# Performance work log

Measured on AMD Instinct MI355X. Metric: run time of the kernel, lower is better.

Reference implementation:

```python
import jax, jax.numpy as jnp
import numpy as np

D_MODEL = 256
N_HEADS = 8
HEAD_DIM = D_MODEL // N_HEADS


def setup_inputs() -> dict:
    key = jax.random.key(0)
    k1, k2, k3, k4, k5, k6, k7 = jax.random.split(key, 7)
    B, T, N, D = 4, 32, 32, D_MODEL
    x = jax.random.normal(k1, (B, T, N, D), dtype=jnp.float32)
    bias_features = jax.random.normal(k2, (B, T, N, N, D), dtype=jnp.float32)
    # alive mask, mostly True so rows are rarely fully masked
    mask = jax.random.uniform(k3, (B, T, N)) < 0.9
    s = 1.0 / np.sqrt(D)
    w_qkv = jax.random.normal(k4, (D, 3 * D), dtype=jnp.float32) * s
    b_qkv = jnp.zeros((3 * D,), dtype=jnp.float32)
    w_proj = jax.random.normal(k5, (D, D), dtype=jnp.float32) * s
    b_proj = jnp.zeros((D,), dtype=jnp.float32)
    return {"x": x, "bias_features": bias_features, "mask": mask,
            "w_qkv": w_qkv, "b_qkv": b_qkv, "w_proj": w_proj, "b_proj": b_proj}


def reference(x, bias_features, mask, w_qkv, b_qkv, w_proj, b_proj):
    B, T, N, D = x.shape
    H, Dh = N_HEADS, D // N_HEADS
    Bt = B * T
    xf = x.reshape(Bt, N, D)
    qkv = xf @ w_qkv + b_qkv                       # (Bt, N, 3D)
    q, k, v = jnp.split(qkv, 3, axis=-1)
    q = q.reshape(Bt, N, H, Dh)
    k = k.reshape(Bt, N, H, Dh)
    v = v.reshape(Bt, N, H, Dh)
    b_geo = bias_features.reshape(Bt, N, N, H, Dh)
    k_pair = k[:, None] + b_geo                    # (Bt, N, N, H, Dh)
    v_pair = v[:, None] + b_geo
    # scores: (Bt, H, N, N)
    scores = jnp.einsum('bihd,bijhd->bhij', q, k_pair) * (Dh ** -0.5)
    mask_flat = mask.reshape(Bt, 1, 1, N)
    scores = jnp.where(mask_flat, scores, -jnp.inf)
    max_scores = jnp.max(scores, axis=-1, keepdims=True)
    is_nan_row = max_scores == -jnp.inf
    scores_safe = jnp.where(is_nan_row, 0.0, scores)
    attn = jax.nn.softmax(scores_safe, axis=-1)
    attn = jnp.where(is_nan_row, 0.0, attn)
    out = jnp.einsum('bhij,bijhd->bihd', attn, v_pair).reshape(Bt, N, D)
    out = out.reshape(B, T, N, D)
    return out @ w_proj + b_proj
```

## Files before the change

### kernel.cpp

```cpp
#include <hip/hip_runtime.h>
#include <math.h>

typedef __attribute__((ext_vector_type(8))) short bf16x8;
typedef __attribute__((ext_vector_type(4))) short bf16x4;
typedef __attribute__((ext_vector_type(4))) float f32x4;

__device__ inline ushort f2bf(float f) {
    union { float f; uint u; } v; v.f = f;
    uint u = v.u;
    return (ushort)((u + 0x7fff + ((u >> 16) & 1)) >> 16);
}
__device__ inline float bf2f(ushort u) {
    union { uint u; float f; } v; v.u = ((uint)u) << 16; return v.f;
}

template<int BM, int BN, int WGM, int WGN, int MODE>
__global__ __launch_bounds__(WGM * WGN * 64) void gemm_fused(
    const void* __restrict__ Ap, const float* __restrict__ Bw, int ldb,
    const float* __restrict__ bias,
    void* __restrict__ C0, void* __restrict__ C1, void* __restrict__ C2,
    int K, int N)
{
    constexpr int BK = 32;
    constexpr int NT = WGM * WGN * 64;
    constexpr int WM = BM / (WGM * 16);
    constexpr int WN = BN / (WGN * 16);

    __shared__ ushort As[BM * BK];
    __shared__ ushort Bs[BN * BK];

    const int tid = threadIdx.x;
    const int lane = tid & 63, wid = tid >> 6;
    const int wm = wid / WGN, wn = wid % WGN;
    const int row0 = blockIdx.y * BM, col0 = blockIdx.x * BN;
    const int frow = lane & 15, fg = lane >> 4;

    f32x4 acc[WM][WN] = {};

    for (int k0 = 0; k0 < K; k0 += BK) {
        if constexpr (MODE == 0) {
            #pragma unroll
            for (int ci = tid; ci < BM * 8; ci += NT) {
                int r = ci >> 3, kq = ci & 7, g = kq >> 1;
                float4 v = *(const float4*)((const float*)Ap + (size_t)(row0 + r) * K + k0 + kq * 4);
                bf16x4 o;
                o[0] = (short)f2bf(v.x); o[1] = (short)f2bf(v.y);
                o[2] = (short)f2bf(v.z); o[3] = (short)f2bf(v.w);
                *(bf16x4*)&As[r * 32 + ((g ^ ((r >> 1) & 3)) << 3) + (kq & 1) * 4] = o;
            }
        } else {
            #pragma unroll
            for (int ci = tid; ci < BM * 4; ci += NT) {
                int r = ci >> 2, g = ci & 3;
                bf16x8 v = *(const bf16x8*)((const ushort*)Ap + (size_t)(row0 + r) * K + k0 + g * 8);
                *(bf16x8*)&As[r * 32 + ((g ^ ((r >> 1) & 3)) << 3)] = v;
            }
        }
        #pragma unroll
        for (int ci = tid; ci < BN * 8; ci += NT) {
            int kk = ci & 31, n4 = ci >> 5;
            float4 v = *(const float4*)&Bw[(size_t)(k0 + kk) * ldb + col0 + n4 * 4];
            float vv[4] = {v.x, v.y, v.z, v.w};
            #pragma unroll
            for (int e = 0; e < 4; ++e) {
                int n = n4 * 4 + e;
                Bs[n * 32 + (((kk >> 3) ^ ((n >> 1) & 3)) << 3) + (kk & 7)] = f2bf(vv[e]);
            }
        }
        __syncthreads();

        bf16x8 af[WM], bfr[WN];
        #pragma unroll
        for (int m = 0; m < WM; ++m) {
            int r = (wm * WM + m) * 16 + frow;
            af[m] = *(const bf16x8*)&As[r * 32 + ((fg ^ ((r >> 1) & 3)) << 3)];
        }
        #pragma unroll
        for (int n = 0; n < WN; ++n) {
            int r = (wn * WN + n) * 16 + frow;
            bfr[n] = *(const bf16x8*)&Bs[r * 32 + ((fg ^ ((r >> 1) & 3)) << 3)];
        }
        #pragma unroll
        for (int m = 0; m < WM; ++m)
            #pragma unroll
            for (int n = 0; n < WN; ++n)
                acc[m][n] = __builtin_amdgcn_mfma_f32_16x16x32_bf16(
                    af[m], bfr[n], acc[m][n], 0, 0, 0);
        __syncthreads();
    }

    #pragma unroll
    for (int n = 0; n < WN; ++n) {
        int gcol = col0 + (wn * WN + n) * 16 + frow;
        float bv = bias[gcol];
        if constexpr (MODE == 0) {
            int b = gcol >> 8, c = gcol & 255;
            ushort* dst = (b == 0) ? (ushort*)C0 : (b == 1) ? (ushort*)C1 : (ushort*)C2;
            #pragma unroll
            for (int m = 0; m < WM; ++m) {
                int grow0 = row0 + (wm * WM + m) * 16 + fg * 4;
                #pragma unroll
                for (int r = 0; r < 4; ++r)
                    dst[(size_t)(grow0 + r) * 256 + c] = f2bf(acc[m][n][r] + bv);
            }
        } else {
            float* dst = (float*)C0;
            #pragma unroll
            for (int m = 0; m < WM; ++m) {
                int grow0 = row0 + (wm * WM + m) * 16 + fg * 4;
                #pragma unroll
                for (int r = 0; r < 4; ++r)
                    dst[(size_t)(grow0 + r) * N + gcol] = acc[m][n][r] + bv;
            }
        }
    }
}

__global__ __launch_bounds__(256) void relattn_kernel(
    const ushort* __restrict__ qb, const ushort* __restrict__ kb,
    const ushort* __restrict__ vb, const float* __restrict__ bias,
    const int* __restrict__ mask, ushort* __restrict__ attn_out)
{
    __shared__ ushort bias_lds[8192];
    __shared__ float p_lds[256];

    const int blk = blockIdx.x;
    const int bt = blk >> 5;
    const int tid = threadIdx.x;
    const float* bsrc = bias + (size_t)blk * 8192;

    #pragma unroll
    for (int it = 0; it < 8; ++it) {
        int idx4 = it * 256 + tid;
        float4 v = *(const float4*)(bsrc + (size_t)idx4 * 4);
        int j = idx4 >> 6;
        int c = (idx4 & 63) >> 1;
        int half = idx4 & 1;
        bf16x4 o;
        o[0] = (short)f2bf(v.x); o[1] = (short)f2bf(v.y);
        o[2] = (short)f2bf(v.z); o[3] = (short)f2bf(v.w);
        *(bf16x4*)&bias_lds[j * 256 + ((c ^ (j & 7)) << 3) + half * 4] = o;
    }
    __syncthreads();

    const int j = tid & 31, h = tid >> 5;
    const ushort* qrow = qb + (size_t)blk * 256 + h * 32;
    const ushort* krow = kb + (size_t)(bt * 32 + j) * 256 + h * 32;

    float s = 0.f;
    #pragma unroll
    for (int it = 0; it < 4; ++it) {
        bf16x8 q8 = *(const bf16x8*)(qrow + it * 8);
        bf16x8 k8 = *(const bf16x8*)(krow + it * 8);
        int c = h * 4 + it;
        bf16x8 b8 = *(const bf16x8*)&bias_lds[j * 256 + ((c ^ (j & 7)) << 3)];
        #pragma unroll
        for (int e = 0; e < 8; ++e)
            s += bf2f((ushort)q8[e]) * (bf2f((ushort)k8[e]) + bf2f((ushort)b8[e]));
    }
    s *= 0.17677669529663687f;

    const bool alive = (mask[bt * 32 + j] != 0);
    s = alive ? s : -__builtin_inff();

    float m = s;
    #pragma unroll
    for (int off = 16; off; off >>= 1) m = fmaxf(m, __shfl_xor(m, off));
    const bool dead = (m == -__builtin_inff());
    float p = alive ? __expf(s - m) : 0.f;
    float l = p;
    #pragma unroll
    for (int off = 16; off; off >>= 1) l += __shfl_xor(l, off);
    p_lds[tid] = dead ? 0.f : p / l;
    __syncthreads();

    const ushort* vcol = vb + (size_t)bt * 8192 + tid;
    const int hbase = tid & 0xE0;
    const int cc = tid >> 3, dlo = tid & 7;
    float o = 0.f;
    #pragma unroll
    for (int jj = 0; jj < 32; ++jj) {
        float pv = p_lds[hbase | jj];
        float vv = bf2f(vcol[(size_t)jj * 256]);
        float bb = bf2f(bias_lds[jj * 256 + ((cc ^ (jj & 7)) << 3) + dlo]);
        o += pv * (vv + bb);
    }
    attn_out[(size_t)blk * 256 + tid] = f2bf(o);
}

extern "C" void kernel_launch(void* const* d_in, const int* in_sizes, int n_in,
                              void* d_out, int out_size, void* d_ws, size_t ws_size,
                              hipStream_t stream) {
    const float* x      = (const float*)d_in[0];
    const float* bias_f = (const float*)d_in[1];
    const int*   mask   = (const int*)d_in[2];
    const float* w_qkv  = (const float*)d_in[3];
    const float* b_qkv  = (const float*)d_in[4];
    const float* w_proj = (const float*)d_in[5];
    const float* b_proj = (const float*)d_in[6];
    float* out = (float*)d_out;

    ushort* qb = (ushort*)d_ws;
    ushort* kb = qb + (size_t)4096 * 256;
    ushort* vb = kb + (size_t)4096 * 256;
    ushort* ao = vb + (size_t)4096 * 256;

    gemm_fused<64, 64, 2, 2, 0><<<dim3(12, 64), 256, 0, stream>>>(
        x, w_qkv, 768, b_qkv, qb, kb, vb, 256, 768);

    relattn_kernel<<<4096, 256, 0, stream>>>(qb, kb, vb, bias_f, mask, ao);

    gemm_fused<32, 64, 1, 4, 1><<<dim3(4, 128), 256, 0, stream>>>(
        ao, w_proj, 256, b_proj, out, nullptr, nullptr, 256, 256);
}
```

Baseline: 58.33 us.

## Make relative attention wave-local: per-wave bias slabs, shuffles instead of block barriers

The attention kernel now has each wave own two heads and stage only its 64-channel slice of the bias tile into a private LDS slab. This removes both block-wide barriers, and softmax weights are broadcast with wave shuffles instead of going through shared memory. The P·V loop is split into four independent accumulators for more ILP. The trade-off is that bias loads become strided scalar global reads (one float per lane per row) instead of float4 loads, which may reduce load efficiency. The slab also relies on wave-level ordering between LDS writes and reads without an explicit barrier.

```diff
diff --git a/kernel.cpp b/kernel.cpp
--- a/kernel.cpp
+++ b/kernel.cpp
@@ -121,46 +121,53 @@
     const ushort* __restrict__ vb, const float* __restrict__ bias,
     const int* __restrict__ mask, ushort* __restrict__ attn_out)
 {
-    __shared__ ushort bias_lds[8192];
-    __shared__ float p_lds[256];
+    __shared__ ushort slab[4][32 * 64];
 
     const int blk = blockIdx.x;
     const int bt = blk >> 5;
     const int tid = threadIdx.x;
-    const float* bsrc = bias + (size_t)blk * 8192;
-
-    #pragma unroll
-    for (int it = 0; it < 8; ++it) {
-        int idx4 = it * 256 + tid;
-        float4 v = *(const float4*)(bsrc + (size_t)idx4 * 4);
-        int j = idx4 >> 6;
-        int c = (idx4 & 63) >> 1;
-        int half = idx4 & 1;
-        bf16x4 o;
-        o[0] = (short)f2bf(v.x); o[1] = (short)f2bf(v.y);
-        o[2] = (short)f2bf(v.z); o[3] = (short)f2bf(v.w);
-        *(bf16x4*)&bias_lds[j * 256 + ((c ^ (j & 7)) << 3) + half * 4] = o;
-    }
-    __syncthreads();
-
-    const int j = tid & 31, h = tid >> 5;
+    const int w = tid >> 6, L = tid & 63;
+    const int hw = L >> 5;
+    const int h = 2 * w + hw;
+    const int jd = L & 31;
+
+    ushort* sl = slab[w];
+
+    const float* bs = bias + (size_t)blk * 8192 + w * 64 + L;
+    #pragma unroll
+    for (int g = 0; g < 4; ++g) {
+        float t0 = bs[(size_t)(g * 8 + 0) * 256];
+        float t1 = bs[(size_t)(g * 8 + 1) * 256];
+        float t2 = bs[(size_t)(g * 8 + 2) * 256];
+        float t3 = bs[(size_t)(g * 8 + 3) * 256];
+        float t4 = bs[(size_t)(g * 8 + 4) * 256];
+        float t5 = bs[(size_t)(g * 8 + 5) * 256];
+        float t6 = bs[(size_t)(g * 8 + 6) * 256];
+        float t7 = bs[(size_t)(g * 8 + 7) * 256];
+        float tt[8] = {t0, t1, t2, t3, t4, t5, t6, t7};
+        #pragma unroll
+        for (int r = 0; r < 8; ++r) {
+            int j = g * 8 + r;
+            sl[j * 64 + ((((L >> 3) ^ (j & 7)) << 3) | (L & 7))] = f2bf(tt[r]);
+        }
+    }
+
     const ushort* qrow = qb + (size_t)blk * 256 + h * 32;
-    const ushort* krow = kb + (size_t)(bt * 32 + j) * 256 + h * 32;
-
+    const ushort* krow = kb + (size_t)(bt * 32 + jd) * 256 + h * 32;
     float s = 0.f;
     #pragma unroll
-    for (int it = 0; it < 4; ++it) {
-        bf16x8 q8 = *(const bf16x8*)(qrow + it * 8);
-        bf16x8 k8 = *(const bf16x8*)(krow + it * 8);
-        int c = h * 4 + it;
-        bf16x8 b8 = *(const bf16x8*)&bias_lds[j * 256 + ((c ^ (j & 7)) << 3)];
+    for (int t = 0; t < 4; ++t) {
+        bf16x8 q8 = *(const bf16x8*)(qrow + t * 8);
+        bf16x8 k8 = *(const bf16x8*)(krow + t * 8);
+        int cc = hw * 4 + t;
+        bf16x8 b8 = *(const bf16x8*)&sl[jd * 64 + ((cc ^ (jd & 7)) << 3)];
         #pragma unroll
         for (int e = 0; e < 8; ++e)
             s += bf2f((ushort)q8[e]) * (bf2f((ushort)k8[e]) + bf2f((ushort)b8[e]));
     }
     s *= 0.17677669529663687f;
 
-    const bool alive = (mask[bt * 32 + j] != 0);
+    const bool alive = (mask[bt * 32 + jd] != 0);
     s = alive ? s : -__builtin_inff();
 
     float m = s;
@@ -171,21 +178,32 @@
     float l = p;
     #pragma unroll
     for (int off = 16; off; off >>= 1) l += __shfl_xor(l, off);
-    p_lds[tid] = dead ? 0.f : p / l;
-    __syncthreads();
-
-    const ushort* vcol = vb + (size_t)bt * 8192 + tid;
-    const int hbase = tid & 0xE0;
-    const int cc = tid >> 3, dlo = tid & 7;
-    float o = 0.f;
-    #pragma unroll
-    for (int jj = 0; jj < 32; ++jj) {
-        float pv = p_lds[hbase | jj];
-        float vv = bf2f(vcol[(size_t)jj * 256]);
-        float bb = bf2f(bias_lds[jj * 256 + ((cc ^ (jj & 7)) << 3) + dlo]);
-        o += pv * (vv + bb);
-    }
-    attn_out[(size_t)blk * 256 + tid] = f2bf(o);
+    float pn = dead ? 0.f : p / l;
+
+    const ushort* vcol = vb + (size_t)bt * 8192 + w * 64 + L;
+    const int half = L & 32;
+    float o0 = 0.f, o1 = 0.f, o2 = 0.f, o3 = 0.f;
+    #pragma unroll
+    for (int jq = 0; jq < 8; ++jq) {
+        int j0 = jq * 4;
+        float pa = __shfl(pn, half | (j0 + 0));
+        float pb = __shfl(pn, half | (j0 + 1));
+        float pc = __shfl(pn, half | (j0 + 2));
+        float pd = __shfl(pn, half | (j0 + 3));
+        float va = bf2f(vcol[(size_t)(j0 + 0) * 256]);
+        float vbv = bf2f(vcol[(size_t)(j0 + 1) * 256]);
+        float vc = bf2f(vcol[(size_t)(j0 + 2) * 256]);
+        float vd = bf2f(vcol[(size_t)(j0 + 3) * 256]);
+        float ba = bf2f(sl[(j0 + 0) * 64 + ((((L >> 3) ^ ((j0 + 0) & 7)) << 3) | (L & 7))]);
+        float bb = bf2f(sl[(j0 + 1) * 64 + ((((L >> 3) ^ ((j0 + 1) & 7)) << 3) | (L & 7))]);
+        float bc = bf2f(sl[(j0 + 2) * 64 + ((((L >> 3) ^ ((j0 + 2) & 7)) << 3) | (L & 7))]);
+        float bd = bf2f(sl[(j0 + 3) * 64 + ((((L >> 3) ^ ((j0 + 3) & 7)) << 3) | (L & 7))]);
+        o0 += pa * (va + ba);
+        o1 += pb * (vbv + bb);
+        o2 += pc * (vc + bc);
+        o3 += pd * (vd + bd);
+    }
+    attn_out[(size_t)blk * 256 + w * 64 + L] = f2bf((o0 + o1) + (o2 + o3));
 }
 
 extern "C" void kernel_launch(void* const* d_in, const int* in_sizes, int n_in,
```

Result: no change. 57.99 us (-0.6%).
